# Performance work log

Hardware: AMD Instinct MI355X
Metric: run time of the kernel (lower is better)

## Reference

```python
import jax, jax.numpy as jnp
import numpy as np

B, N, D = 32, 1024, 64   # batch, n_agents, obs_dim (n_agent_inputs)
H, OUT, K = 128, 8, 16   # gnn_hidden_dim, n_agent_outputs, k_neighbours


def setup_inputs() -> dict:
    key = jax.random.key(0)
    k0, k1, k2, k3 = jax.random.split(key, 4)
    s = lambda d: 1.0 / np.sqrt(d)
    return {
        "agent_observations": jax.random.normal(k0, (B, N, D), jnp.float32),
        "W1": jax.random.normal(k1, (D, H), jnp.float32) * s(D),
        "b1": jnp.zeros((H,), jnp.float32),
        "W2": jax.random.normal(k2, (H, H), jnp.float32) * s(H),
        "b2": jnp.zeros((H,), jnp.float32),
        "W_out": jax.random.normal(k3, (H, OUT), jnp.float32) * s(H),
        "b_out": jnp.zeros((OUT,), jnp.float32),
    }


def _forward(obs, W1, b1, W2, b2, W_out, b_out):
    Bs, Nn, _ = obs.shape
    # active-agent mask, as in torch forward: any nonzero feature
    mask = jnp.any(obs != 0.0, axis=2)               # [B, N] bool
    maskf = mask.astype(obs.dtype)
    pos = obs[:, :, 0:2]                              # pos_indices = slice(0, 2)
    # squared pairwise distances (same ordering as cdist p=2, avoids sqrt-at-0 grads)
    diff = pos[:, :, None, :] - pos[:, None, :, :]    # [B, N, N, 2]
    d2 = jnp.sum(diff * diff, axis=-1)                # [B, N, N]
    valid = mask[:, :, None] & mask[:, None, :]
    d2 = jnp.where(valid, d2, jnp.inf)
    # k+1 nearest (self has distance 0 -> first column), drop self
    _, idx = jax.lax.top_k(-d2, K + 1)                # [B, N, K+1]
    nbr = idx[:, :, 1:]                               # targets of edges source->neighbor
    bidx = jnp.arange(Bs)[:, None, None]
    w = jnp.broadcast_to(maskf[:, :, None], nbr.shape)  # edge valid iff source active
    # GCN symmetric norm (gcn_norm re-adds self-loops on top of the module's
    # explicit self-loops -> diagonal weight 2). deg = in-degree incl. 2*self.
    deg = jnp.zeros((Bs, Nn), obs.dtype).at[bidx, nbr].add(w) + 2.0 * maskf
    dinv = jnp.where(deg > 0, jax.lax.rsqrt(jnp.where(deg > 0, deg, 1.0)), 0.0)

    def gcn(h, W, b):
        y = h @ W                                     # [B, N, H']
        # per-edge messages dinv[src] * y[src], scattered into targets
        z = (dinv[:, :, None] * y)[:, :, None, :] * w[..., None]  # [B, N, K, H']
        agg = jnp.zeros_like(y).at[bidx, nbr].add(z)  # sum over in-edges
        out = dinv[:, :, None] * agg + 2.0 * (dinv * dinv)[:, :, None] * y
        return jnp.tanh(out + b)                      # activation_class = Tanh

    h = gcn(obs, W1, b1)
    h = gcn(h, W2, b2)
    out = h @ W_out + b_out                           # output_mlp
    return out * maskf[:, :, None]                    # zeros for inactive agents


def reference(agent_observations, W1, b1, W2, b2, W_out, b_out):
    return _forward(agent_observations, W1, b1, W2, b2, W_out, b_out)
```

## Files before the change

### kernel.cpp

```cpp
#include <hip/hip_runtime.h>
#include <hip/hip_bf16.h>
#include <math.h>

#define BB 32
#define NN 1024
#define DD 64
#define HH 128
#define KK 16
#define OD 8
#define M_TOT (BB*NN)

typedef unsigned long long u64;

static __device__ __forceinline__ int d2b7(float d2) {
  int v = (int)(__float_as_uint(d2) >> 22) - 200;
  v = v < 0 ? 0 : v;
  return v > 126 ? 126 : v;
}

template <int CIN, bool EMIT_MASK>
__global__ __launch_bounds__(512) void k_gemm(const float* __restrict__ X,
                                              const float* __restrict__ W,
                                              float* __restrict__ Y,
                                              float* __restrict__ maskf,
                                              int* __restrict__ degi,
                                              float2* __restrict__ pxy) {
  __shared__ float Ws[32 * HH];
  __shared__ float Xt[32 * 68];
  __shared__ int rowflag[64];
  __shared__ float2 praw[64];
  const int t = threadIdx.x;
  const size_t rowbase = (size_t)blockIdx.x * 64;

  if (EMIT_MASK && t < 64) rowflag[t] = 0;

  const int c4 = (t & 31) * 4;
  const int r4 = (t >> 5) * 4;

  float acc[4][4] = {{0.f}};

  for (int k0 = 0; k0 < CIN; k0 += 32) {
    __syncthreads();
    {
      const float4* Wt4 = (const float4*)(W + (size_t)k0 * HH);
      ((float4*)Ws)[t]       = Wt4[t];
      ((float4*)Ws)[t + 512] = Wt4[t + 512];
    }
    {
      const int row = t >> 3;
      const int kq  = t & 7;
      float4 v = *(const float4*)(X + (rowbase + row) * CIN + k0 + kq * 4);
      if (EMIT_MASK) {
        if (v.x != 0.f || v.y != 0.f || v.z != 0.f || v.w != 0.f)
          rowflag[row] = 1;
        if (k0 == 0 && kq == 0) praw[row] = make_float2(v.x, v.y);
      }
      Xt[(kq * 4 + 0) * 68 + row] = v.x;
      Xt[(kq * 4 + 1) * 68 + row] = v.y;
      Xt[(kq * 4 + 2) * 68 + row] = v.z;
      Xt[(kq * 4 + 3) * 68 + row] = v.w;
    }
    __syncthreads();
#pragma unroll
    for (int k = 0; k < 32; ++k) {
      const float4 xa = *(const float4*)&Xt[k * 68 + r4];
      const float4 wb = *(const float4*)&Ws[k * HH + c4];
      acc[0][0] += xa.x * wb.x; acc[0][1] += xa.x * wb.y; acc[0][2] += xa.x * wb.z; acc[0][3] += xa.x * wb.w;
      acc[1][0] += xa.y * wb.x; acc[1][1] += xa.y * wb.y; acc[1][2] += xa.y * wb.z; acc[1][3] += xa.y * wb.w;
      acc[2][0] += xa.z * wb.x; acc[2][1] += xa.z * wb.y; acc[2][2] += xa.z * wb.z; acc[2][3] += xa.z * wb.w;
      acc[3][0] += xa.w * wb.x; acc[3][1] += xa.w * wb.y; acc[3][2] += xa.w * wb.z; acc[3][3] += xa.w * wb.w;
    }
  }
#pragma unroll
  for (int i = 0; i < 4; ++i)
    *(float4*)(Y + (rowbase + r4 + i) * HH + c4) =
        make_float4(acc[i][0], acc[i][1], acc[i][2], acc[i][3]);

  if (EMIT_MASK && t < 64) {
    const size_t gr = rowbase + t;
    const int any = rowflag[t];
    maskf[gr] = any ? 1.f : 0.f;
    degi[gr] = 0;
    const float inf = __builtin_inff();
    pxy[gr] = any ? praw[t] : make_float2(inf, inf);
  }
}

__global__ __launch_bounds__(256) void k_topk(const float2* __restrict__ pxy,
                                              const float* __restrict__ maskf,
                                              int* __restrict__ nbr,
                                              int* __restrict__ degi) {
  __shared__ float2 pls[NN];
  __shared__ u64 lst[16][64];
  __shared__ int dcnt[16];
  __shared__ int ccnt[16];

  const int b = blockIdx.x;
  const int t = threadIdx.x;
  const int rl = t >> 4;
  const int s  = t & 15;
  const int row = blockIdx.y * 16 + rl;
  const size_t r = (size_t)b * NN + row;

  {
    const float4* src = (const float4*)(pxy + (size_t)b * NN);
    float4* dst = (float4*)pls;
    dst[t] = src[t];
    dst[t + 256] = src[t + 256];
  }
  if (s == 0) { dcnt[rl] = 0; ccnt[rl] = 0; }
  __syncthreads();

  const bool valid = (maskf[r] != 0.f);
  const float2 pi = pls[row];
  const float xi = pi.x, yi = pi.y;
  const float4* pls4 = (const float4*)pls;

  u64 cc[8];
  if (valid) {
#pragma unroll
    for (int q = 0; q < 8; ++q) {
      unsigned lo = 0, hiw = 0;
#pragma unroll
      for (int ii = 0; ii < 4; ++ii) {
        const int i = q * 4 + ii;
        const int p = (i + s) & 31;
        const float4 pr = pls4[s * 32 + p];
        const float dx0 = __fsub_rn(xi, pr.x), dy0 = __fsub_rn(yi, pr.y);
        const float d20 = __fadd_rn(__fmul_rn(dx0, dx0), __fmul_rn(dy0, dy0));
        const float dx1 = __fsub_rn(xi, pr.z), dy1 = __fsub_rn(yi, pr.w);
        const float d21 = __fadd_rn(__fmul_rn(dx1, dx1), __fmul_rn(dy1, dy1));
        const unsigned pb = (unsigned)d2b7(d20) | ((unsigned)d2b7(d21) << 8);
        if (ii == 0) lo |= pb;
        else if (ii == 1) lo |= pb << 16;
        else if (ii == 2) hiw |= pb;
        else hiw |= pb << 16;
      }
      cc[q] = (u64)lo | ((u64)hiw << 32);
    }
    if (s == (row >> 6)) {
      const int c = row & 63;
      const int i = ((c >> 1) - s) & 31;
      const int q_ = i >> 2;
      const int u_ = 2 * (i & 3) + (c & 1);
      const u64 pb = 0x7Full << (8 * u_);
#pragma unroll
      for (int q = 0; q < 8; ++q) if (q == q_) cc[q] |= pb;
    }
  } else {
#pragma unroll
    for (int q = 0; q < 8; ++q) cc[q] = 0x7F7F7F7F7F7F7F7Full;
  }

  int lo = 0, hi = 126, ndef = 0;
#pragma unroll
  for (int it = 0; it < 7; ++it) {
    const int mid = (lo + hi) >> 1;
    const u64 K = (u64)(unsigned)(128 + mid) * 0x0101010101010101ull;
    int c = 0;
#pragma unroll
    for (int q = 0; q < 8; ++q)
      c += __popcll((K - cc[q]) & 0x8080808080808080ull);
#pragma unroll
    for (int off = 1; off < 16; off <<= 1)
      c += __shfl_xor(c, off, 16);
    if (c >= 16) hi = mid;
    else { lo = mid + 1; ndef = c; }
  }
  const int Bstar = lo;
  int need = 16 - ndef;

  int cem = 0;
  if (valid) {
    const u64 Klo = (u64)(unsigned)(127 + Bstar) * 0x0101010101010101ull;
    const u64 Khi = Klo + 0x0101010101010101ull;
#pragma unroll
    for (int q = 0; q < 8; ++q) {
      const u64 w = cc[q];
      const u64 mLE = (Khi - w) & 0x8080808080808080ull;
      if (mLE) {
        const u64 mLT = (Klo - w) & 0x8080808080808080ull;
#pragma unroll
        for (int u = 0; u < 8; ++u) {
          const u64 bit = 0x80ull << (8 * u);
          if (mLE & bit) {
            const int i = q * 4 + (u >> 1);
            const int j = s * 64 + (((i + s) & 31) << 1) + (u & 1);
            if (mLT & bit) {
              const int sl = atomicAdd(&dcnt[rl], 1);
              nbr[r * KK + sl] = j;
              atomicAdd(&degi[b * NN + j], 1);
            } else {
              const float2 p = pls[j];
              const float dx = __fsub_rn(xi, p.x);
              const float dy = __fsub_rn(yi, p.y);
              const float d2 = __fadd_rn(__fmul_rn(dx, dx), __fmul_rn(dy, dy));
              const int sl = atomicAdd(&ccnt[rl], 1);
              if (sl < 64) lst[rl][sl] = ((u64)__float_as_uint(d2) << 10) | (unsigned)j;
              ++cem;
            }
          }
        }
      }
    }
  }
  __syncthreads();

  int cn = cem;
#pragma unroll
  for (int off = 1; off < 16; off <<= 1) cn += __shfl_xor(cn, off, 16);
  cn = cn < 64 ? cn : 64;
  if (!valid) { cn = 0; need = 0; }

  u64 k0 = (s      < cn) ? lst[rl][s]      : ~0ull;
  u64 k1 = (s + 16 < cn) ? lst[rl][s + 16] : ~0ull;
  u64 k2 = (s + 32 < cn) ? lst[rl][s + 32] : ~0ull;
  u64 k3 = (s + 48 < cn) ? lst[rl][s + 48] : ~0ull;

  int e = 0;
  while (__any(e < need)) {
    u64 m01 = k0 < k1 ? k0 : k1;
    u64 m23 = k2 < k3 ? k2 : k3;
    u64 m = m01 < m23 ? m01 : m23;
#pragma unroll
    for (int off = 1; off < 16; off <<= 1) {
      const u64 o = __shfl_xor(m, off, 16);
      m = o < m ? o : m;
    }
    if (e < need) {
      if (k0 == m) k0 = ~0ull;
      else if (k1 == m) k1 = ~0ull;
      else if (k2 == m) k2 = ~0ull;
      else if (k3 == m) k3 = ~0ull;
      if (s == 0) {
        const int j = (int)(m & (u64)(NN - 1));
        nbr[r * KK + ndef + e] = j;
        atomicAdd(&degi[b * NN + j], 1);
      }
    }
    ++e;
  }
}

__global__ __launch_bounds__(1024) void k_graph(const int* __restrict__ degi,
                                                const float* __restrict__ maskf,
                                                const int* __restrict__ nbr,
                                                int* __restrict__ cur,
                                                float* __restrict__ dinv,
                                                int2* __restrict__ rev) {
  __shared__ int wsum[16];
  __shared__ int lcur[NN];
  const int b = blockIdx.x, t = threadIdx.x;
  const int lane = t & 63, w = t >> 6;
  const int r = b * NN + t;
  const int d = degi[r];
  int x = d;
#pragma unroll
  for (int off = 1; off < 64; off <<= 1) {
    int y = __shfl_up(x, off, 64);
    if (lane >= off) x += y;
  }
  if (lane == 63) wsum[w] = x;

  const float m = maskf[r];
  const float deg = (float)d + 2.f * m;
  const float dv = (deg > 0.f) ? (1.f / sqrtf(deg)) : 0.f;
  dinv[r] = dv;
  const float sv = dv * m;

  __syncthreads();
  if (w == 0) {
    int v = (lane < 16) ? wsum[lane] : 0;
#pragma unroll
    for (int off = 1; off < 16; off <<= 1) {
      int y = __shfl_up(v, off, 64);
      if (lane >= off) v += y;
    }
    if (lane < 16) wsum[lane] = v;
  }
  __syncthreads();
  const int start = b * (NN * KK) + (w ? wsum[w - 1] : 0) + x - d;
  lcur[t] = start;
  cur[r] = start;
  __syncthreads();

  if (m != 0.f) {
    const int sb = __float_as_int(sv);
    const int4* n4 = (const int4*)(nbr + (size_t)r * KK);
#pragma unroll
    for (int q = 0; q < 4; ++q) {
      int4 v = n4[q];
      int nb[4] = {v.x, v.y, v.z, v.w};
#pragma unroll
      for (int u = 0; u < 4; ++u) {
        const int pos = atomicAdd(&lcur[nb[u]], 1);
        rev[pos] = make_int2(r, sb);
      }
    }
  }
}

__global__ __launch_bounds__(1024) void k_gcnc(const float* __restrict__ y,
                                               const float* __restrict__ dinv,
                                               const int* __restrict__ degi,
                                               const int* __restrict__ cur,
                                               const int2* __restrict__ rev,
                                               const float* __restrict__ bias,
                                               float* __restrict__ hout) {
  __shared__ float4 ych[NN * 2];
  const int b = blockIdx.x;
  const int c0 = blockIdx.y * 8;
  const int t = threadIdx.x;

  {
    const float* yb = y + (size_t)b * NN * HH + c0;
#pragma unroll
    for (int k = 0; k < 2; ++k) {
      const int idx = t + k * 1024;
      const int rowq = idx >> 1, cq = idx & 1;
      ych[rowq * 2 + ((cq + rowq) & 1)] =
          *(const float4*)(yb + (size_t)rowq * HH + cq * 4);
    }
  }
  __syncthreads();

  const int r = b * NN + t;
  const int cnt = degi[r];
  const int off = cur[r];
  const float di = dinv[r];

  float4 a0 = make_float4(0.f, 0.f, 0.f, 0.f);
  float4 a1 = a0;
  for (int e = 0; e < cnt; ++e) {
    const int2 ed = rev[off + e];
    const int sl = ed.x & (NN - 1);
    const float se = __int_as_float(ed.y);
    const int base = sl * 2;
    const float4 y0 = ych[base + (sl & 1)];
    const float4 y1 = ych[base + ((sl + 1) & 1)];
    a0.x += se * y0.x; a0.y += se * y0.y; a0.z += se * y0.z; a0.w += se * y0.w;
    a1.x += se * y1.x; a1.y += se * y1.y; a1.z += se * y1.z; a1.w += se * y1.w;
  }

  const int nb2 = t * 2;
  const float4 s0 = ych[nb2 + (t & 1)];
  const float4 s1 = ych[nb2 + ((t + 1) & 1)];
  const float4 b0 = *(const float4*)(bias + c0);
  const float4 b1 = *(const float4*)(bias + c0 + 4);
  const float t2 = 2.f * di * di;

  float4 h0, h1;
  h0.x = tanhf(di * a0.x + t2 * s0.x + b0.x);
  h0.y = tanhf(di * a0.y + t2 * s0.y + b0.y);
  h0.z = tanhf(di * a0.z + t2 * s0.z + b0.z);
  h0.w = tanhf(di * a0.w + t2 * s0.w + b0.w);
  h1.x = tanhf(di * a1.x + t2 * s1.x + b1.x);
  h1.y = tanhf(di * a1.y + t2 * s1.y + b1.y);
  h1.z = tanhf(di * a1.z + t2 * s1.z + b1.z);
  h1.w = tanhf(di * a1.w + t2 * s1.w + b1.w);

  float4* hrow = (float4*)(hout + (size_t)r * HH + c0);
  hrow[0] = h0; hrow[1] = h1;
}

__global__ __launch_bounds__(256) void k_out(const float* __restrict__ h,
                                             const float* __restrict__ Wo,
                                             const float* __restrict__ bo,
                                             const float* __restrict__ maskf,
                                             float* __restrict__ out) {
  __shared__ float Ws[HH * OD];
  __shared__ float bs[OD];
  const int t = threadIdx.x;
  for (int q = t; q < HH * OD / 4; q += 256) ((float4*)Ws)[q] = ((const float4*)Wo)[q];
  if (t < OD) bs[t] = bo[t];
  __syncthreads();

  const size_t r = (size_t)blockIdx.x * 256 + t;
  const float4* hrow = (const float4*)(h + r * HH);
  float acc[OD];
#pragma unroll
  for (int o = 0; o < OD; ++o) acc[o] = 0.f;

#pragma unroll 4
  for (int q = 0; q < HH / 4; ++q) {
    const float4 hv = hrow[q];
    const float* w = &Ws[(q * 4) * OD];
#pragma unroll
    for (int o = 0; o < OD; ++o) acc[o] += hv.x * w[o];
#pragma unroll
    for (int o = 0; o < OD; ++o) acc[o] += hv.y * w[OD + o];
#pragma unroll
    for (int o = 0; o < OD; ++o) acc[o] += hv.z * w[2 * OD + o];
#pragma unroll
    for (int o = 0; o < OD; ++o) acc[o] += hv.w * w[3 * OD + o];
  }
  const float mf = maskf[r];
  float4* orow = (float4*)(out + r * OD);
  orow[0] = make_float4((acc[0] + bs[0]) * mf, (acc[1] + bs[1]) * mf,
                        (acc[2] + bs[2]) * mf, (acc[3] + bs[3]) * mf);
  orow[1] = make_float4((acc[4] + bs[4]) * mf, (acc[5] + bs[5]) * mf,
                        (acc[6] + bs[6]) * mf, (acc[7] + bs[7]) * mf);
}

extern "C" void kernel_launch(void* const* d_in, const int* in_sizes, int n_in,
                              void* d_out, int out_size, void* d_ws, size_t ws_size,
                              hipStream_t stream) {
  (void)in_sizes; (void)n_in; (void)out_size; (void)ws_size;
  const float* obs = (const float*)d_in[0];
  const float* W1  = (const float*)d_in[1];
  const float* b1  = (const float*)d_in[2];
  const float* W2  = (const float*)d_in[3];
  const float* b2  = (const float*)d_in[4];
  const float* Wo  = (const float*)d_in[5];
  const float* bo  = (const float*)d_in[6];
  float* out = (float*)d_out;

  char* ws = (char*)d_ws;
  float* maskf = (float*)(ws);
  int*   degi  = (int*)  (ws + (size_t)(128 << 10));
  float* dinv  = (float*)(ws + (size_t)(256 << 10));
  int*   cur   = (int*)  (ws + (size_t)(384 << 10));
  float2* pxy  = (float2*)(ws + (size_t)(512 << 10));
  int*   nbr   = (int*)  (ws + (size_t)(1u << 20));
  int2*  rev   = (int2*) (ws + (size_t)(3u << 20));
  float* ybuf  = (float*)(ws + (size_t)(7u << 20));
  float* hbuf  = (float*)(ws + (size_t)(23u << 20));

  k_gemm<DD, true><<<M_TOT / 64, 512, 0, stream>>>(obs, W1, ybuf, maskf, degi, pxy);
  k_topk<<<dim3(BB, NN / 16), 256, 0, stream>>>(pxy, maskf, nbr, degi);
  k_graph<<<BB, 1024, 0, stream>>>(degi, maskf, nbr, cur, dinv, rev);
  k_gcnc<<<dim3(BB, HH / 8), 1024, 0, stream>>>(ybuf, dinv, degi, cur, rev, b1, hbuf);
  k_gemm<HH, false><<<M_TOT / 64, 512, 0, stream>>>(hbuf, W2, ybuf, nullptr, nullptr, nullptr);
  k_gcnc<<<dim3(BB, HH / 8), 1024, 0, stream>>>(ybuf, dinv, degi, cur, rev, b2, hbuf);
  k_out<<<M_TOT / 256, 256, 0, stream>>>(hbuf, Wo, bo, maskf, out);
}
```

Baseline: 135.1 us.

## Use one wavefront per row in top-k and split graph build into scan and fill

The top-k kernel now assigns a full 64-lane wavefront to each query row instead of 16 lanes, so each lane holds 16 candidate distances instead of 64. The binary search and the final selection now reduce across the whole wave, and the grid becomes four times larger. The reverse-edge construction is split out of the per-batch 1024-thread kernel into a scan kernel plus a separate grid-wide fill kernel that uses global atomics on a cursor copy. This spreads the work across more blocks for parallelism, at the cost of an extra launch, more global atomics, and a larger top-k block count that repeats the shared-memory position load.

```diff
diff --git a/kernel.cpp b/kernel.cpp
--- a/kernel.cpp
+++ b/kernel.cpp
@@ -91,15 +91,15 @@
                                               int* __restrict__ nbr,
                                               int* __restrict__ degi) {
   __shared__ float2 pls[NN];
-  __shared__ u64 lst[16][64];
-  __shared__ int dcnt[16];
-  __shared__ int ccnt[16];
+  __shared__ u64 lst[4][64];
+  __shared__ int dcnt[4];
+  __shared__ int ccnt[4];
 
   const int b = blockIdx.x;
   const int t = threadIdx.x;
-  const int rl = t >> 4;
-  const int s  = t & 15;
-  const int row = blockIdx.y * 16 + rl;
+  const int w = t >> 6;
+  const int l = t & 63;
+  const int row = blockIdx.y * 4 + w;
   const size_t r = (size_t)b * NN + row;
 
   {
@@ -108,7 +108,7 @@
     dst[t] = src[t];
     dst[t + 256] = src[t + 256];
   }
-  if (s == 0) { dcnt[rl] = 0; ccnt[rl] = 0; }
+  if (l == 0) { dcnt[w] = 0; ccnt[w] = 0; }
   __syncthreads();
 
   const bool valid = (maskf[r] != 0.f);
@@ -116,16 +116,16 @@
   const float xi = pi.x, yi = pi.y;
   const float4* pls4 = (const float4*)pls;
 
-  u64 cc[8];
+  u64 cc[2];
   if (valid) {
 #pragma unroll
-    for (int q = 0; q < 8; ++q) {
+    for (int q = 0; q < 2; ++q) {
       unsigned lo = 0, hiw = 0;
 #pragma unroll
       for (int ii = 0; ii < 4; ++ii) {
         const int i = q * 4 + ii;
-        const int p = (i + s) & 31;
-        const float4 pr = pls4[s * 32 + p];
+        const int p = (i + l) & 7;
+        const float4 pr = pls4[l * 8 + p];
         const float dx0 = __fsub_rn(xi, pr.x), dy0 = __fsub_rn(yi, pr.y);
         const float d20 = __fadd_rn(__fmul_rn(dx0, dx0), __fmul_rn(dy0, dy0));
         const float dx1 = __fsub_rn(xi, pr.z), dy1 = __fsub_rn(yi, pr.w);
@@ -138,18 +138,16 @@
       }
       cc[q] = (u64)lo | ((u64)hiw << 32);
     }
-    if (s == (row >> 6)) {
-      const int c = row & 63;
-      const int i = ((c >> 1) - s) & 31;
-      const int q_ = i >> 2;
+    if (l == (row >> 4)) {
+      const int c = row & 15;
+      const int i = ((c >> 1) - l) & 7;
       const int u_ = 2 * (i & 3) + (c & 1);
       const u64 pb = 0x7Full << (8 * u_);
-#pragma unroll
-      for (int q = 0; q < 8; ++q) if (q == q_) cc[q] |= pb;
+      if (i < 4) cc[0] |= pb; else cc[1] |= pb;
     }
   } else {
-#pragma unroll
-    for (int q = 0; q < 8; ++q) cc[q] = 0x7F7F7F7F7F7F7F7Full;
+    cc[0] = 0x7F7F7F7F7F7F7F7Full;
+    cc[1] = 0x7F7F7F7F7F7F7F7Full;
   }
 
   int lo = 0, hi = 126, ndef = 0;
@@ -157,13 +155,11 @@
   for (int it = 0; it < 7; ++it) {
     const int mid = (lo + hi) >> 1;
     const u64 K = (u64)(unsigned)(128 + mid) * 0x0101010101010101ull;
-    int c = 0;
-#pragma unroll
-    for (int q = 0; q < 8; ++q)
-      c += __popcll((K - cc[q]) & 0x8080808080808080ull);
-#pragma unroll
-    for (int off = 1; off < 16; off <<= 1)
-      c += __shfl_xor(c, off, 16);
+    int c = __popcll((K - cc[0]) & 0x8080808080808080ull)
+          + __popcll((K - cc[1]) & 0x8080808080808080ull);
+#pragma unroll
+    for (int off = 1; off < 64; off <<= 1)
+      c += __shfl_xor(c, off, 64);
     if (c >= 16) hi = mid;
     else { lo = mid + 1; ndef = c; }
   }
@@ -175,19 +171,19 @@
     const u64 Klo = (u64)(unsigned)(127 + Bstar) * 0x0101010101010101ull;
     const u64 Khi = Klo + 0x0101010101010101ull;
 #pragma unroll
-    for (int q = 0; q < 8; ++q) {
-      const u64 w = cc[q];
-      const u64 mLE = (Khi - w) & 0x8080808080808080ull;
+    for (int q = 0; q < 2; ++q) {
+      const u64 ww = cc[q];
+      const u64 mLE = (Khi - ww) & 0x8080808080808080ull;
       if (mLE) {
-        const u64 mLT = (Klo - w) & 0x8080808080808080ull;
+        const u64 mLT = (Klo - ww) & 0x8080808080808080ull;
 #pragma unroll
         for (int u = 0; u < 8; ++u) {
           const u64 bit = 0x80ull << (8 * u);
           if (mLE & bit) {
             const int i = q * 4 + (u >> 1);
-            const int j = s * 64 + (((i + s) & 31) << 1) + (u & 1);
+            const int j = l * 16 + (((i + l) & 7) << 1) + (u & 1);
             if (mLT & bit) {
-              const int sl = atomicAdd(&dcnt[rl], 1);
+              const int sl = atomicAdd(&dcnt[w], 1);
               nbr[r * KK + sl] = j;
               atomicAdd(&degi[b * NN + j], 1);
             } else {
@@ -195,8 +191,8 @@
               const float dx = __fsub_rn(xi, p.x);
               const float dy = __fsub_rn(yi, p.y);
               const float d2 = __fadd_rn(__fmul_rn(dx, dx), __fmul_rn(dy, dy));
-              const int sl = atomicAdd(&ccnt[rl], 1);
-              if (sl < 64) lst[rl][sl] = ((u64)__float_as_uint(d2) << 10) | (unsigned)j;
+              const int sl = atomicAdd(&ccnt[w], 1);
+              if (sl < 64) lst[w][sl] = ((u64)__float_as_uint(d2) << 10) | (unsigned)j;
               ++cem;
             }
           }
@@ -208,48 +204,35 @@
 
   int cn = cem;
 #pragma unroll
-  for (int off = 1; off < 16; off <<= 1) cn += __shfl_xor(cn, off, 16);
+  for (int off = 1; off < 64; off <<= 1) cn += __shfl_xor(cn, off, 64);
   cn = cn < 64 ? cn : 64;
   if (!valid) { cn = 0; need = 0; }
 
-  u64 k0 = (s      < cn) ? lst[rl][s]      : ~0ull;
-  u64 k1 = (s + 16 < cn) ? lst[rl][s + 16] : ~0ull;
-  u64 k2 = (s + 32 < cn) ? lst[rl][s + 32] : ~0ull;
-  u64 k3 = (s + 48 < cn) ? lst[rl][s + 48] : ~0ull;
-
-  int e = 0;
-  while (__any(e < need)) {
-    u64 m01 = k0 < k1 ? k0 : k1;
-    u64 m23 = k2 < k3 ? k2 : k3;
-    u64 m = m01 < m23 ? m01 : m23;
-#pragma unroll
-    for (int off = 1; off < 16; off <<= 1) {
-      const u64 o = __shfl_xor(m, off, 16);
+  u64 k0 = (l < cn) ? lst[w][l] : ~0ull;
+
+  for (int e = 0; e < need; ++e) {
+    u64 m = k0;
+#pragma unroll
+    for (int off = 1; off < 64; off <<= 1) {
+      const u64 o = __shfl_xor(m, off, 64);
       m = o < m ? o : m;
     }
-    if (e < need) {
-      if (k0 == m) k0 = ~0ull;
-      else if (k1 == m) k1 = ~0ull;
-      else if (k2 == m) k2 = ~0ull;
-      else if (k3 == m) k3 = ~0ull;
-      if (s == 0) {
-        const int j = (int)(m & (u64)(NN - 1));
-        nbr[r * KK + ndef + e] = j;
-        atomicAdd(&degi[b * NN + j], 1);
-      }
-    }
-    ++e;
-  }
-}
-
-__global__ __launch_bounds__(1024) void k_graph(const int* __restrict__ degi,
-                                                const float* __restrict__ maskf,
-                                                const int* __restrict__ nbr,
-                                                int* __restrict__ cur,
-                                                float* __restrict__ dinv,
-                                                int2* __restrict__ rev) {
+    if (k0 == m) k0 = ~0ull;
+    if (l == 0) {
+      const int j = (int)(m & (u64)(NN - 1));
+      nbr[r * KK + ndef + e] = j;
+      atomicAdd(&degi[b * NN + j], 1);
+    }
+  }
+}
+
+__global__ __launch_bounds__(1024) void k_scan(const int* __restrict__ degi,
+                                               const float* __restrict__ maskf,
+                                               int* __restrict__ cur,
+                                               int* __restrict__ curw,
+                                               float* __restrict__ dinv,
+                                               float* __restrict__ sbuf) {
   __shared__ int wsum[16];
-  __shared__ int lcur[NN];
   const int b = blockIdx.x, t = threadIdx.x;
   const int lane = t & 63, w = t >> 6;
   const int r = b * NN + t;
@@ -266,7 +249,7 @@
   const float deg = (float)d + 2.f * m;
   const float dv = (deg > 0.f) ? (1.f / sqrtf(deg)) : 0.f;
   dinv[r] = dv;
-  const float sv = dv * m;
+  sbuf[r] = dv * m;
 
   __syncthreads();
   if (w == 0) {
@@ -280,22 +263,28 @@
   }
   __syncthreads();
   const int start = b * (NN * KK) + (w ? wsum[w - 1] : 0) + x - d;
-  lcur[t] = start;
   cur[r] = start;
-  __syncthreads();
-
-  if (m != 0.f) {
-    const int sb = __float_as_int(sv);
-    const int4* n4 = (const int4*)(nbr + (size_t)r * KK);
-#pragma unroll
-    for (int q = 0; q < 4; ++q) {
-      int4 v = n4[q];
-      int nb[4] = {v.x, v.y, v.z, v.w};
-#pragma unroll
-      for (int u = 0; u < 4; ++u) {
-        const int pos = atomicAdd(&lcur[nb[u]], 1);
-        rev[pos] = make_int2(r, sb);
-      }
+  curw[r] = start;
+}
+
+__global__ __launch_bounds__(256) void k_fill(const int* __restrict__ nbr,
+                                              const float* __restrict__ maskf,
+                                              const float* __restrict__ sbuf,
+                                              int* __restrict__ curw,
+                                              int2* __restrict__ rev) {
+  const int r = blockIdx.x * 256 + threadIdx.x;
+  if (maskf[r] == 0.f) return;
+  const int bbase = r & ~(NN - 1);
+  const int sb = __float_as_int(sbuf[r]);
+  const int4* n4 = (const int4*)(nbr + (size_t)r * KK);
+#pragma unroll
+  for (int q = 0; q < 4; ++q) {
+    int4 v = n4[q];
+    int nb[4] = {v.x, v.y, v.z, v.w};
+#pragma unroll
+    for (int u = 0; u < 4; ++u) {
+      const int pos = atomicAdd(&curw[bbase + nb[u]], 1);
+      rev[pos] = make_int2(r, sb);
     }
   }
 }
@@ -421,14 +410,17 @@
   float* dinv  = (float*)(ws + (size_t)(256 << 10));
   int*   cur   = (int*)  (ws + (size_t)(384 << 10));
   float2* pxy  = (float2*)(ws + (size_t)(512 << 10));
+  int*   curw  = (int*)  (ws + (size_t)(768 << 10));
+  float* sbuf  = (float*)(ws + (size_t)(896 << 10));
   int*   nbr   = (int*)  (ws + (size_t)(1u << 20));
   int2*  rev   = (int2*) (ws + (size_t)(3u << 20));
   float* ybuf  = (float*)(ws + (size_t)(7u << 20));
   float* hbuf  = (float*)(ws + (size_t)(23u << 20));
 
   k_gemm<DD, true><<<M_TOT / 64, 512, 0, stream>>>(obs, W1, ybuf, maskf, degi, pxy);
-  k_topk<<<dim3(BB, NN / 16), 256, 0, stream>>>(pxy, maskf, nbr, degi);
-  k_graph<<<BB, 1024, 0, stream>>>(degi, maskf, nbr, cur, dinv, rev);
+  k_topk<<<dim3(BB, NN / 4), 256, 0, stream>>>(pxy, maskf, nbr, degi);
+  k_scan<<<BB, 1024, 0, stream>>>(degi, maskf, cur, curw, dinv, sbuf);
+  k_fill<<<M_TOT / 256, 256, 0, stream>>>(nbr, maskf, sbuf, curw, rev);
   k_gcnc<<<dim3(BB, HH / 8), 1024, 0, stream>>>(ybuf, dinv, degi, cur, rev, b1, hbuf);
   k_gemm<HH, false><<<M_TOT / 64, 512, 0, stream>>>(hbuf, W2, ybuf, nullptr, nullptr, nullptr);
   k_gcnc<<<dim3(BB, HH / 8), 1024, 0, stream>>>(ybuf, dinv, degi, cur, rev, b2, hbuf);
```

New measurement: 155.8 us. 1.15x slower.
